# Performance work log

Measured on AMD Instinct MI355X. Metric: run time of the kernel, lower is better.

The kernel has to match this reference:

```python
import jax, jax.numpy as jnp
import numpy as np

HIDDEN = 512
EPS = 1e-5  # BatchNorm1d default eps


def _ligru_layer(x, Ww, Wu, gamma, beta):
    # x: [T, B, F] time-major. Bidirectional: stack flipped copy along batch.
    x2 = jnp.concatenate([x, x[::-1]], axis=1)          # [T, 2B, F]
    w = jnp.einsum('tbf,gf->tbg', x2, Ww)               # [T, 2B, 2H]
    # BatchNorm over flattened (T*2B) rows, per feature (training-mode stats)
    mean = jnp.mean(w, axis=(0, 1))
    var = jnp.mean((w - mean) ** 2, axis=(0, 1))
    w = gamma * (w - mean) * jax.lax.rsqrt(var + EPS) + beta

    H = Wu.shape[1]
    h0 = jnp.zeros((w.shape[1], H), dtype=w.dtype)

    def step(h, wk):
        gates = wk + h @ Wu.T                            # [2B, 2H]
        at, zt = gates[:, :H], gates[:, H:]
        zt = jax.nn.sigmoid(zt)
        hcand = jax.nn.relu(at)                          # drop_mask == 1 (dropout=0)
        h = zt * h + (1.0 - zt) * hcand
        return h, h

    _, h = jax.lax.scan(step, h0, w)                     # [T, 2B, H]
    B = x.shape[1]
    h_f, h_b = h[:, :B], h[:, B:]
    return jnp.concatenate([h_f, h_b[::-1]], axis=2)     # [T, B, 2H]


def setup_inputs() -> dict:
    key = jax.random.key(0)
    ks = jax.random.split(key, 7)
    B, T, F, H = 16, 500, 240, HIDDEN
    x = jax.random.normal(ks[0], (B, T, F), dtype=jnp.float32)
    # layer 0: in=F, layer 1: in=2H (bidirectional output)
    Ww0 = jax.random.normal(ks[1], (2 * H, F), dtype=jnp.float32) / np.sqrt(F)
    Wu0 = jax.random.normal(ks[2], (2 * H, H), dtype=jnp.float32) / np.sqrt(H)
    Ww1 = jax.random.normal(ks[3], (2 * H, 2 * H), dtype=jnp.float32) / np.sqrt(2 * H)
    Wu1 = jax.random.normal(ks[4], (2 * H, H), dtype=jnp.float32) / np.sqrt(H)
    g0 = jnp.ones((2 * H,), jnp.float32)
    b0 = jnp.zeros((2 * H,), jnp.float32)
    g1 = jnp.ones((2 * H,), jnp.float32)
    b1 = jnp.zeros((2 * H,), jnp.float32)
    return {"x": x, "Ww0": Ww0, "Wu0": Wu0, "g0": g0, "b0": b0,
            "Ww1": Ww1, "Wu1": Wu1, "g1": g1, "b1": b1}


def reference(x, Ww0, Wu0, g0, b0, Ww1, Wu1, g1, b1):
    h = x.transpose(1, 0, 2)                             # [T, B, F]
    h = _ligru_layer(h, Ww0, Wu0, g0, b0)                # [T, B, 2H]
    h = _ligru_layer(h, Ww1, Wu1, g1, b1)                # [T, B, 2H]
    return h.transpose(1, 0, 2)                          # [B, T, 2H]
```

## Files before the change

kernel.cpp:

```cpp
#include <hip/hip_runtime.h>
#include <math.h>
#include <stdint.h>

#define TT 500
#define B2 32
#define FF 240
#define HH 512
#define G2 1024
#define MROWS (TT*B2)
#define REC_WGS 8
#define FLAG_STRIDE 16
#define FLAGS_PER_LAYER (TT*8*FLAG_STRIDE)

typedef __attribute__((ext_vector_type(8))) short bf16x8;
typedef __attribute__((ext_vector_type(4))) short bf16x4;
typedef __attribute__((ext_vector_type(4))) float f32x4;
typedef unsigned long long u64;

typedef __attribute__((address_space(1))) const unsigned int GU32;
typedef __attribute__((address_space(3))) unsigned int LU32;

static __device__ __forceinline__ unsigned short f2bf(float f) {
    union { float f; unsigned u; } v; v.f = f;
    unsigned r = v.u + 0x7FFFu + ((v.u >> 16) & 1u);
    return (unsigned short)(r >> 16);
}

static __device__ __forceinline__ void gload_lds16(const void* g, void* l) {
    __builtin_amdgcn_global_load_lds((GU32*)g, (LU32*)l, 16, 0, 0);
}

__global__ void zero_cnt(unsigned int* cnt) {
    cnt[blockIdx.x * 256 + threadIdx.x] = 0u;
}

__global__ __launch_bounds__(256)
void cvt_a0(const float* __restrict__ x, unsigned short* __restrict__ A0)
{
    const int idx = blockIdx.x * 256 + threadIdx.x;
    const int m = idx >> 5;
    const int k = (idx & 31) * 8;
    const int t = m >> 5, b2 = m & 31;
    bf16x8 o = {0,0,0,0,0,0,0,0};
    if (k < FF) {
        const float* p = (b2 < 16)
            ? x + ((size_t)(b2 * TT + t)) * FF + k
            : x + ((size_t)((b2 - 16) * TT + (TT - 1 - t))) * FF + k;
        f32x4 a = *(const f32x4*)p;
        f32x4 b = *(const f32x4*)(p + 4);
        #pragma unroll
        for (int j = 0; j < 4; ++j) { o[j] = (short)f2bf(a[j]); o[4+j] = (short)f2bf(b[j]); }
    }
    *(bf16x8*)(A0 + (size_t)m * 256 + k) = o;
}

template<int Kin, int Kout>
__global__ __launch_bounds__(256)
void cvt_pad(const float* __restrict__ src, unsigned short* __restrict__ dst)
{
    const int idx = blockIdx.x * 256 + threadIdx.x;
    const int r = idx / (Kout / 8);
    const int k = (idx % (Kout / 8)) * 8;
    bf16x8 o = {0,0,0,0,0,0,0,0};
    if (k + 8 <= Kin) {
        f32x4 a = *(const f32x4*)(src + (size_t)r * Kin + k);
        f32x4 b = *(const f32x4*)(src + (size_t)r * Kin + k + 4);
        #pragma unroll
        for (int j = 0; j < 4; ++j) { o[j] = (short)f2bf(a[j]); o[4+j] = (short)f2bf(b[j]); }
    }
    *(bf16x8*)(dst + (size_t)r * Kout + k) = o;
}

template<int K>
__global__ __launch_bounds__(256, 2)
void mfma_gemm(const unsigned short* __restrict__ A,
               const unsigned short* __restrict__ B,
               float* __restrict__ C)
{
    __shared__ alignas(16) char As[16384];
    __shared__ alignas(16) char Bs[16384];
    const int tid = threadIdx.x;
    const int wv = tid >> 6, l = tid & 63, l15 = l & 15, lg = l >> 4;
    const int m0 = blockIdx.x * 128, n0 = blockIdx.y * 128;
    const int wr = wv >> 1, wc = wv & 1;
    f32x4 acc[4][4];
    #pragma unroll
    for (int i = 0; i < 4; ++i)
        #pragma unroll
        for (int j = 0; j < 4; ++j) acc[i][j] = (f32x4){0.f, 0.f, 0.f, 0.f};

    for (int ko = 0; ko < K; ko += 64) {
        #pragma unroll
        for (int i = 0; i < 4; ++i) {
            const int ch = tid + i * 256;
            const int row = ch >> 3, q = ch & 7;
            const int kb = (q * 16) ^ ((row & 7) << 4);
            gload_lds16(A + (size_t)(m0 + row) * K + ko + (kb >> 1), As + ch * 16);
            gload_lds16(B + (size_t)(n0 + row) * K + ko + (kb >> 1), Bs + ch * 16);
        }
        __syncthreads();
        #pragma unroll
        for (int ks = 0; ks < 2; ++ks) {
            bf16x8 af[4], bf[4];
            #pragma unroll
            for (int ib = 0; ib < 4; ++ib) {
                const int r = wr * 64 + ib * 16 + l15;
                const int sz = (r & 7) << 4;
                const int kb0 = ks * 64 + lg * 8;
                bf16x4 lo = *(const bf16x4*)(As + r * 128 + (kb0 ^ sz));
                bf16x4 hi = *(const bf16x4*)(As + r * 128 + ((kb0 + 32) ^ sz));
                bf16x8 f;
                f[0]=lo[0]; f[1]=lo[1]; f[2]=lo[2]; f[3]=lo[3];
                f[4]=hi[0]; f[5]=hi[1]; f[6]=hi[2]; f[7]=hi[3];
                af[ib] = f;
            }
            #pragma unroll
            for (int jb = 0; jb < 4; ++jb) {
                const int r = wc * 64 + jb * 16 + l15;
                const int sz = (r & 7) << 4;
                const int kb0 = ks * 64 + lg * 8;
                bf16x4 lo = *(const bf16x4*)(Bs + r * 128 + (kb0 ^ sz));
                bf16x4 hi = *(const bf16x4*)(Bs + r * 128 + ((kb0 + 32) ^ sz));
                bf16x8 f;
                f[0]=lo[0]; f[1]=lo[1]; f[2]=lo[2]; f[3]=lo[3];
                f[4]=hi[0]; f[5]=hi[1]; f[6]=hi[2]; f[7]=hi[3];
                bf[jb] = f;
            }
            #pragma unroll
            for (int ib = 0; ib < 4; ++ib)
                #pragma unroll
                for (int jb = 0; jb < 4; ++jb)
                    acc[ib][jb] = __builtin_amdgcn_mfma_f32_16x16x32_bf16(af[ib], bf[jb], acc[ib][jb], 0, 0, 0);
        }
        __syncthreads();
    }
    #pragma unroll
    for (int ib = 0; ib < 4; ++ib)
        #pragma unroll
        for (int jb = 0; jb < 4; ++jb)
            #pragma unroll
            for (int rr = 0; rr < 4; ++rr)
                C[(size_t)(m0 + wr * 64 + ib * 16 + lg * 4 + rr) * G2 +
                  (n0 + wc * 64 + jb * 16 + l15)] = acc[ib][jb][rr];
}

__global__ __launch_bounds__(256)
void stats_partial(const float* __restrict__ w, float* __restrict__ partS,
                   float* __restrict__ partQ)
{
    const int col = blockIdx.x * 256 + threadIdx.x;
    const int row0 = blockIdx.y * 128;
    float s = 0.f, q = 0.f;
    for (int r = 0; r < 128; ++r) {
        float v = w[(size_t)(row0 + r) * G2 + col];
        s += v; q += v * v;
    }
    partS[blockIdx.y * G2 + col] = s;
    partQ[blockIdx.y * G2 + col] = q;
}

__global__ __launch_bounds__(256)
void stats_final(const float* __restrict__ partS, const float* __restrict__ partQ,
                 const float* __restrict__ gamma, const float* __restrict__ beta,
                 float* __restrict__ scale, float* __restrict__ shift)
{
    const int col = blockIdx.x * 256 + threadIdx.x;
    float s = 0.f, q = 0.f;
    for (int i = 0; i < 125; ++i) { s += partS[i * G2 + col]; q += partQ[i * G2 + col]; }
    const float mean = s * (1.f / 16000.f);
    float var = q * (1.f / 16000.f) - mean * mean;
    var = fmaxf(var, 0.f);
    const float sc = gamma[col] * rsqrtf(var + 1e-5f);
    scale[col] = sc;
    shift[col] = beta[col] - mean * sc;
}

template<int LAYER>
__global__ __launch_bounds__(512, 2)
void rec_kernel(const float* __restrict__ w, const float* __restrict__ scale,
                const float* __restrict__ shift, const float* __restrict__ Wu,
                void* __restrict__ outp, u64* __restrict__ hx,
                unsigned int* __restrict__ flags)
{
    __shared__ alignas(16) char hbuf[2][16384];

    const int g   = blockIdx.x;
    const int d   = g >> 2;
    const int q   = g & 3;
    const int tid = threadIdx.x;
    const int wv  = tid >> 6;
    const int l   = tid & 63;
    const int l15 = l & 15;
    const int lg  = l >> 4;
    const int jcol = 128 * q + 16 * wv + l15;

    u64* hx_d = hx + (size_t)d * 4096;

    bf16x8 bfa[16], bfz[16];
    {
        const float* pa = Wu + (size_t)jcol * HH;
        const float* pz = Wu + (size_t)(HH + jcol) * HH;
        #pragma unroll
        for (int ks = 0; ks < 16; ++ks) {
            f32x4 a0 = *(const f32x4*)(pa + ks * 32 + lg * 4);
            f32x4 a1 = *(const f32x4*)(pa + ks * 32 + lg * 4 + 16);
            f32x4 z0 = *(const f32x4*)(pz + ks * 32 + lg * 4);
            f32x4 z1 = *(const f32x4*)(pz + ks * 32 + lg * 4 + 16);
            bf16x8 fa, fz;
            #pragma unroll
            for (int j = 0; j < 4; ++j) {
                fa[j]     = (short)f2bf(a0[j]);
                fa[4 + j] = (short)f2bf(a1[j]);
                fz[j]     = (short)f2bf(z0[j]);
                fz[4 + j] = (short)f2bf(z1[j]);
            }
            bfa[ks] = fa; bfz[ks] = fz;
        }
    }
    const float scl_a = scale[jcol],      sh_a = shift[jcol];
    const float scl_z = scale[HH + jcol], sh_z = shift[HH + jcol];

    float hold[4] = {0.f, 0.f, 0.f, 0.f};

    for (int i = tid; i < 2048; i += 512) ((uint4*)hbuf)[i] = make_uint4(0, 0, 0, 0);
    __syncthreads();

    const int grow = tid >> 5, guc = tid & 31;
    const int gswz = (grow & 7) << 4;

    for (int t = 0; t < TT; ++t) {
        const int p = t & 1;

        float wa_[4], wz_[4];
        #pragma unroll
        for (int r = 0; r < 4; ++r) {
            const int b2 = d * 16 + lg * 4 + r;
            const float* wp = w + ((size_t)t * B2 + b2) * G2 + jcol;
            wa_[r] = wp[0];
            wz_[r] = wp[HH];
        }

        if (t > 0) {
            {
                const unsigned int* fl = flags +
                    ((size_t)(t - 1) * 8 + d * 4) * FLAG_STRIDE;
                unsigned v = 1u;
                do {
                    if (l < 4)
                        v = __hip_atomic_load(fl + l * FLAG_STRIDE, __ATOMIC_RELAXED,
                                              __HIP_MEMORY_SCOPE_AGENT);
                    if (__any(v == 0u)) __builtin_amdgcn_s_sleep(1); else break;
                } while (true);
            }
            const u64* src = hx_d + (size_t)(p ^ 1) * 2048;
            u64 vv[3];
            #pragma unroll
            for (int i = 0; i < 3; ++i) {
                const int sw = i + (i >= q);
                vv[i] = __hip_atomic_load(src + sw * 512 + grow * 32 + guc,
                                          __ATOMIC_RELAXED, __HIP_MEMORY_SCOPE_AGENT);
            }
            char* db = hbuf[p] + grow * 1024;
            #pragma unroll
            for (int i = 0; i < 3; ++i) {
                const int sw = i + (i >= q);
                *(u64*)(db + ((sw * 256 + guc * 8) ^ gswz)) = vv[i];
            }
            __syncthreads();
        }

        f32x4 aacc = {0.f, 0.f, 0.f, 0.f};
        f32x4 zacc = {0.f, 0.f, 0.f, 0.f};
        const int arow = l15;
        const char* rbase = hbuf[p] + arow * 1024;
        const int swz = (arow & 7) << 4;
        #pragma unroll
        for (int ks = 0; ks < 16; ++ks) {
            const int off0 = ks * 64 + lg * 8;
            bf16x4 h0 = *(const bf16x4*)(rbase + (off0 ^ swz));
            bf16x4 h1 = *(const bf16x4*)(rbase + ((off0 + 32) ^ swz));
            bf16x8 af;
            af[0] = h0[0]; af[1] = h0[1]; af[2] = h0[2]; af[3] = h0[3];
            af[4] = h1[0]; af[5] = h1[1]; af[6] = h1[2]; af[7] = h1[3];
            aacc = __builtin_amdgcn_mfma_f32_16x16x32_bf16(af, bfa[ks], aacc, 0, 0, 0);
            zacc = __builtin_amdgcn_mfma_f32_16x16x32_bf16(af, bfz[ks], zacc, 0, 0, 0);
        }

        #pragma unroll
        for (int r = 0; r < 4; ++r) {
            const int b  = lg * 4 + r;
            const int b2 = d * 16 + b;
            const float aval = scl_a * wa_[r] + sh_a + aacc[r];
            const float zval = scl_z * wz_[r] + sh_z + zacc[r];
            const float zt = 1.f / (1.f + __expf(-zval));
            const float hn = zt * hold[r] + (1.f - zt) * fmaxf(aval, 0.f);
            hold[r] = hn;
            const unsigned short hb = f2bf(hn);
            if (LAYER == 0) {
                unsigned short* A1 = (unsigned short*)outp;
                const int cc = jcol + (d == 0 ? 0 : HH);
                const int r1 = t * B2 + b2;
                const int r2 = (TT - 1 - t) * B2 + (d == 0 ? b2 + 16 : b2 - 16);
                A1[(size_t)r1 * G2 + cc] = hb;
                A1[(size_t)r2 * G2 + cc] = hb;
            } else {
                float* po = (float*)outp;
                const int bb = (d == 0) ? b2 : b2 - 16;
                const int tt = (d == 0) ? t : (TT - 1 - t);
                po[((size_t)bb * TT + tt) * G2 + jcol + (d == 0 ? 0 : HH)] = hn;
            }
            if (t < TT - 1)
                *(unsigned short*)(hbuf[p ^ 1] + b * 1024 +
                                   ((jcol * 2) ^ ((b & 7) << 4))) = hb;
        }

        if (t < TT - 1) {
            __syncthreads();
            {
                const u64 v = *(const u64*)(hbuf[p ^ 1] + grow * 1024 +
                                            ((256 * q + guc * 8) ^ gswz));
                __hip_atomic_store(hx_d + (size_t)p * 2048 + q * 512 + grow * 32 + guc,
                                   v, __ATOMIC_RELAXED, __HIP_MEMORY_SCOPE_AGENT);
            }
            __syncthreads();
            if (tid == 0)
                __hip_atomic_fetch_add(flags + ((size_t)t * 8 + d * 4 + q) * FLAG_STRIDE,
                                       1u, __ATOMIC_RELAXED, __HIP_MEMORY_SCOPE_AGENT);
        }
    }
}

extern "C" void kernel_launch(void* const* d_in, const int* in_sizes, int n_in,
                              void* d_out, int out_size, void* d_ws, size_t ws_size,
                              hipStream_t stream)
{
    const float* x   = (const float*)d_in[0];
    const float* Ww0 = (const float*)d_in[1];
    const float* Wu0 = (const float*)d_in[2];
    const float* g0  = (const float*)d_in[3];
    const float* b0  = (const float*)d_in[4];
    const float* Ww1 = (const float*)d_in[5];
    const float* Wu1 = (const float*)d_in[6];
    const float* g1  = (const float*)d_in[7];
    const float* b1  = (const float*)d_in[8];
    float* out = (float*)d_out;

    float* w     = (float*)d_ws;
    float* scr0  = w + (size_t)MROWS * G2;
    float* scr1  = scr0 + (size_t)TT * B2 * HH;
    float* partS = scr1 + (size_t)TT * B2 * HH;
    float* partQ = partS + 125 * G2;
    float* scale = partQ + 125 * G2;
    float* shift = scale + G2;
    unsigned int* flags = (unsigned int*)(shift + G2);
    u64* hx0 = (u64*)(flags + 2 * FLAGS_PER_LAYER);
    u64* hx1 = hx0 + 8192;

    unsigned short* A0b = (unsigned short*)scr0;
    unsigned short* Wwb = (unsigned short*)(scr0 + 3 * 1024 * 1024);
    unsigned short* A1b = (unsigned short*)scr1;

    const size_t needed = ((size_t)MROWS * G2 + 2 * (size_t)TT * B2 * HH +
                           2 * 125 * G2 + 2 * G2) * 4 +
                          (size_t)2 * FLAGS_PER_LAYER * 4 + 16384 * 8;
    if (ws_size < needed) return;

    zero_cnt<<<2 * FLAGS_PER_LAYER / 256, 256, 0, stream>>>(flags);

    cvt_a0<<<2000, 256, 0, stream>>>(x, A0b);
    cvt_pad<240, 256><<<128, 256, 0, stream>>>(Ww0, Wwb);
    mfma_gemm<256><<<dim3(125, 8), 256, 0, stream>>>(A0b, Wwb, w);
    stats_partial<<<dim3(4, 125), 256, 0, stream>>>(w, partS, partQ);
    stats_final<<<4, 256, 0, stream>>>(partS, partQ, g0, b0, scale, shift);
    rec_kernel<0><<<REC_WGS, 512, 0, stream>>>(w, scale, shift, Wu0, A1b, hx0, flags);

    cvt_pad<1024, 1024><<<512, 256, 0, stream>>>(Ww1, Wwb);
    mfma_gemm<1024><<<dim3(125, 8), 256, 0, stream>>>(A1b, Wwb, w);
    stats_partial<<<dim3(4, 125), 256, 0, stream>>>(w, partS, partQ);
    stats_final<<<4, 256, 0, stream>>>(partS, partQ, g1, b1, scale, shift);
    rec_kernel<1><<<REC_WGS, 512, 0, stream>>>(w, scale, shift, Wu1, out, hx1,
                                               flags + FLAGS_PER_LAYER);
}
```

Baseline: 2.479 ms.

## Replace per-step flag counters with parity-tagged hidden-state words in recurrence

Drops the separate flag array and atomic counter handshake between recurrent workgroups. Each published 64-bit hidden-state chunk now carries a parity bit in its lowest bit, and consumers spin on the data words themselves until the expected epoch appears. Each wave also publishes its own slice directly instead of staging through two block barriers, and the global output stores are moved after the publish. This removes a flag round trip and two __syncthreads per step on the serial critical path, at the cost of overwriting the lowest mantissa bit of one bf16 value per word.

```diff
diff --git a/kernel.cpp b/kernel.cpp
--- a/kernel.cpp
+++ b/kernel.cpp
@@ -9,8 +9,6 @@
 #define G2 1024
 #define MROWS (TT*B2)
 #define REC_WGS 8
-#define FLAG_STRIDE 16
-#define FLAGS_PER_LAYER (TT*8*FLAG_STRIDE)
 
 typedef __attribute__((ext_vector_type(8))) short bf16x8;
 typedef __attribute__((ext_vector_type(4))) short bf16x4;
@@ -30,8 +28,8 @@
     __builtin_amdgcn_global_load_lds((GU32*)g, (LU32*)l, 16, 0, 0);
 }
 
-__global__ void zero_cnt(unsigned int* cnt) {
-    cnt[blockIdx.x * 256 + threadIdx.x] = 0u;
+__global__ void init_hx(u64* hx) {
+    hx[blockIdx.x * 256 + threadIdx.x] = 1ull;
 }
 
 __global__ __launch_bounds__(256)
@@ -179,8 +177,7 @@
 __global__ __launch_bounds__(512, 2)
 void rec_kernel(const float* __restrict__ w, const float* __restrict__ scale,
                 const float* __restrict__ shift, const float* __restrict__ Wu,
-                void* __restrict__ outp, u64* __restrict__ hx,
-                unsigned int* __restrict__ flags)
+                void* __restrict__ outp, u64* __restrict__ hx)
 {
     __shared__ alignas(16) char hbuf[2][16384];
 
@@ -227,6 +224,9 @@
 
     const int grow = tid >> 5, guc = tid & 31;
     const int gswz = (grow & 7) << 4;
+    const int prow = l & 15, pu = l >> 4;
+    const int pbyte = 256 * q + 32 * wv + 8 * pu;
+    const int pswz = (prow & 7) << 4;
 
     for (int t = 0; t < TT; ++t) {
         const int p = t & 1;
@@ -241,25 +241,31 @@
         }
 
         if (t > 0) {
-            {
-                const unsigned int* fl = flags +
-                    ((size_t)(t - 1) * 8 + d * 4) * FLAG_STRIDE;
-                unsigned v = 1u;
-                do {
-                    if (l < 4)
-                        v = __hip_atomic_load(fl + l * FLAG_STRIDE, __ATOMIC_RELAXED,
-                                              __HIP_MEMORY_SCOPE_AGENT);
-                    if (__any(v == 0u)) __builtin_amdgcn_s_sleep(1); else break;
-                } while (true);
-            }
             const u64* src = hx_d + (size_t)(p ^ 1) * 2048;
+            const u64 e = (u64)(((t - 1) >> 1) & 1);
             u64 vv[3];
-            #pragma unroll
-            for (int i = 0; i < 3; ++i) {
-                const int sw = i + (i >= q);
-                vv[i] = __hip_atomic_load(src + sw * 512 + grow * 32 + guc,
-                                          __ATOMIC_RELAXED, __HIP_MEMORY_SCOPE_AGENT);
-            }
+            unsigned pend = 7u;
+            do {
+                u64 tmp[3];
+                #pragma unroll
+                for (int i = 0; i < 3; ++i)
+                    if (pend & (1u << i)) {
+                        const int sw = i + (i >= q);
+                        tmp[i] = __hip_atomic_load(src + sw * 512 + grow * 32 + guc,
+                                                   __ATOMIC_RELAXED,
+                                                   __HIP_MEMORY_SCOPE_AGENT);
+                    }
+                unsigned np = 0;
+                #pragma unroll
+                for (int i = 0; i < 3; ++i)
+                    if (pend & (1u << i)) {
+                        if (__all((tmp[i] & 1ull) == e)) vv[i] = tmp[i];
+                        else                              np |= 1u << i;
+                    }
+                if (np) __builtin_amdgcn_s_sleep(1);
+                pend = np;
+            } while (pend);
+
             char* db = hbuf[p] + grow * 1024;
             #pragma unroll
             for (int i = 0; i < 3; ++i) {
@@ -286,18 +292,37 @@
             zacc = __builtin_amdgcn_mfma_f32_16x16x32_bf16(af, bfz[ks], zacc, 0, 0, 0);
         }
 
+        float hn4[4];
         #pragma unroll
         for (int r = 0; r < 4; ++r) {
-            const int b  = lg * 4 + r;
-            const int b2 = d * 16 + b;
+            const int b = lg * 4 + r;
             const float aval = scl_a * wa_[r] + sh_a + aacc[r];
             const float zval = scl_z * wz_[r] + sh_z + zacc[r];
             const float zt = 1.f / (1.f + __expf(-zval));
             const float hn = zt * hold[r] + (1.f - zt) * fmaxf(aval, 0.f);
-            hold[r] = hn;
-            const unsigned short hb = f2bf(hn);
+            hold[r] = hn; hn4[r] = hn;
+            if (t < TT - 1)
+                *(unsigned short*)(hbuf[p ^ 1] + b * 1024 +
+                                   ((jcol * 2) ^ ((b & 7) << 4))) = f2bf(hn);
+        }
+
+        if (t < TT - 1) {
+            __builtin_amdgcn_sched_barrier(0);
+            const u64 v0 = *(const u64*)(hbuf[p ^ 1] + prow * 1024 + (pbyte ^ pswz));
+            const u64 v = (v0 & ~1ull) | (u64)((t >> 1) & 1);
+            __hip_atomic_store(hx_d + (size_t)p * 2048 + q * 512 + prow * 32 + 4 * wv + pu,
+                               v, __ATOMIC_RELAXED, __HIP_MEMORY_SCOPE_AGENT);
+            __builtin_amdgcn_sched_barrier(0);
+        }
+
+        #pragma unroll
+        for (int r = 0; r < 4; ++r) {
+            const int b  = lg * 4 + r;
+            const int b2 = d * 16 + b;
+            const float hn = hn4[r];
             if (LAYER == 0) {
                 unsigned short* A1 = (unsigned short*)outp;
+                const unsigned short hb = f2bf(hn);
                 const int cc = jcol + (d == 0 ? 0 : HH);
                 const int r1 = t * B2 + b2;
                 const int r2 = (TT - 1 - t) * B2 + (d == 0 ? b2 + 16 : b2 - 16);
@@ -309,23 +334,6 @@
                 const int tt = (d == 0) ? t : (TT - 1 - t);
                 po[((size_t)bb * TT + tt) * G2 + jcol + (d == 0 ? 0 : HH)] = hn;
             }
-            if (t < TT - 1)
-                *(unsigned short*)(hbuf[p ^ 1] + b * 1024 +
-                                   ((jcol * 2) ^ ((b & 7) << 4))) = hb;
-        }
-
-        if (t < TT - 1) {
-            __syncthreads();
-            {
-                const u64 v = *(const u64*)(hbuf[p ^ 1] + grow * 1024 +
-                                            ((256 * q + guc * 8) ^ gswz));
-                __hip_atomic_store(hx_d + (size_t)p * 2048 + q * 512 + grow * 32 + guc,
-                                   v, __ATOMIC_RELAXED, __HIP_MEMORY_SCOPE_AGENT);
-            }
-            __syncthreads();
-            if (tid == 0)
-                __hip_atomic_fetch_add(flags + ((size_t)t * 8 + d * 4 + q) * FLAG_STRIDE,
-                                       1u, __ATOMIC_RELAXED, __HIP_MEMORY_SCOPE_AGENT);
         }
     }
 }
@@ -352,8 +360,7 @@
     float* partQ = partS + 125 * G2;
     float* scale = partQ + 125 * G2;
     float* shift = scale + G2;
-    unsigned int* flags = (unsigned int*)(shift + G2);
-    u64* hx0 = (u64*)(flags + 2 * FLAGS_PER_LAYER);
+    u64* hx0 = (u64*)(shift + G2);
     u64* hx1 = hx0 + 8192;
 
     unsigned short* A0b = (unsigned short*)scr0;
@@ -361,23 +368,21 @@
     unsigned short* A1b = (unsigned short*)scr1;
 
     const size_t needed = ((size_t)MROWS * G2 + 2 * (size_t)TT * B2 * HH +
-                           2 * 125 * G2 + 2 * G2) * 4 +
-                          (size_t)2 * FLAGS_PER_LAYER * 4 + 16384 * 8;
+                           2 * 125 * G2 + 2 * G2) * 4 + 16384 * 8;
     if (ws_size < needed) return;
 
-    zero_cnt<<<2 * FLAGS_PER_LAYER / 256, 256, 0, stream>>>(flags);
+    init_hx<<<64, 256, 0, stream>>>(hx0);
 
     cvt_a0<<<2000, 256, 0, stream>>>(x, A0b);
     cvt_pad<240, 256><<<128, 256, 0, stream>>>(Ww0, Wwb);
     mfma_gemm<256><<<dim3(125, 8), 256, 0, stream>>>(A0b, Wwb, w);
     stats_partial<<<dim3(4, 125), 256, 0, stream>>>(w, partS, partQ);
     stats_final<<<4, 256, 0, stream>>>(partS, partQ, g0, b0, scale, shift);
-    rec_kernel<0><<<REC_WGS, 512, 0, stream>>>(w, scale, shift, Wu0, A1b, hx0, flags);
+    rec_kernel<0><<<REC_WGS, 512, 0, stream>>>(w, scale, shift, Wu0, A1b, hx0);
 
     cvt_pad<1024, 1024><<<512, 256, 0, stream>>>(Ww1, Wwb);
     mfma_gemm<1024><<<dim3(125, 8), 256, 0, stream>>>(A1b, Wwb, w);
     stats_partial<<<dim3(4, 125), 256, 0, stream>>>(w, partS, partQ);
     stats_final<<<4, 256, 0, stream>>>(partS, partQ, g1, b1, scale, shift);
-    rec_kernel<1><<<REC_WGS, 512, 0, stream>>>(w, scale, shift, Wu1, out, hx1,
-                                               flags + FLAGS_PER_LAYER);
-}
+    rec_kernel<1><<<REC_WGS, 512, 0, stream>>>(w, scale, shift, Wu1, out, hx1);
+}
```

Result: slower. 2.579 ms (+4.0%).
